# Performance work log

Measured on AMD Instinct MI355X. Metric: run time of the kernel, lower is better.

## Reference

```python
import jax, jax.numpy as jnp
import numpy as np

H = 128
IN = 5
EPS = 1e-5


def lstm(x, Wih, Whh, bih, bhh):
    # x: [B,T,D]; PyTorch gate order i,f,g,o along 4H axis
    B, T, _ = x.shape
    xW = jnp.einsum('btd,gd->btg', x, Wih) + bih + bhh  # [B,T,4H]
    WhhT = Whh.T

    def step(carry, xt):
        h, c = carry
        g = xt + h @ WhhT
        i, f, gg, o = jnp.split(g, 4, axis=-1)
        i = jax.nn.sigmoid(i)
        f = jax.nn.sigmoid(f)
        gg = jnp.tanh(gg)
        o = jax.nn.sigmoid(o)
        c = f * c + i * gg
        h = o * jnp.tanh(c)
        return (h, c), h

    h0 = jnp.zeros((B, H), x.dtype)
    _, hs = jax.lax.scan(step, (h0, h0), jnp.swapaxes(xW, 0, 1))
    return jnp.swapaxes(hs, 0, 1)  # [B,T,H]


def batchnorm(x, gamma, beta):
    # training-mode BN over (batch, time) per channel; x: [B,T,H]
    mean = jnp.mean(x, axis=(0, 1))
    var = jnp.var(x, axis=(0, 1))
    return (x - mean) * (gamma * jax.lax.rsqrt(var + EPS)) + beta


def forward_one(x, Wih1, Whh1, bih1, bhh1, g1, b1, Wih2, Whh2, bih2, bhh2, g2, b2, fcW, fcb):
    out = lstm(x, Wih1, Whh1, bih1, bhh1)
    out = batchnorm(out, g1, b1)
    # dropout is identity (eval / deterministic reference)
    out = lstm(out, Wih2, Whh2, bih2, bhh2)
    out = batchnorm(out, g2, b2)
    emb = out[:, -1, :] @ fcW.T + fcb  # [B,128]
    norm = jnp.sqrt(jnp.sum(emb * emb, axis=1, keepdims=True))
    return emb / jnp.maximum(norm, 1e-12)  # F.normalize p=2


def setup_inputs() -> dict:
    key = jax.random.key(0)
    ks = jax.random.split(key, 20)
    B, T = 512, 128
    s_in = 1.0 / np.sqrt(H)
    d = {
        'a': jax.random.normal(ks[0], (B, T, IN), jnp.float32),
        'p': jax.random.normal(ks[1], (B, T, IN), jnp.float32),
        'n': jax.random.normal(ks[2], (B, T, IN), jnp.float32),
        'Wih1': jax.random.uniform(ks[3], (4 * H, IN), jnp.float32, -s_in, s_in),
        'Whh1': jax.random.uniform(ks[4], (4 * H, H), jnp.float32, -s_in, s_in),
        'bih1': jax.random.uniform(ks[5], (4 * H,), jnp.float32, -s_in, s_in),
        'bhh1': jax.random.uniform(ks[6], (4 * H,), jnp.float32, -s_in, s_in),
        'g1': jnp.ones((H,), jnp.float32),
        'b1': jnp.zeros((H,), jnp.float32),
        'Wih2': jax.random.uniform(ks[7], (4 * H, H), jnp.float32, -s_in, s_in),
        'Whh2': jax.random.uniform(ks[8], (4 * H, H), jnp.float32, -s_in, s_in),
        'bih2': jax.random.uniform(ks[9], (4 * H,), jnp.float32, -s_in, s_in),
        'bhh2': jax.random.uniform(ks[10], (4 * H,), jnp.float32, -s_in, s_in),
        'g2': jnp.ones((H,), jnp.float32),
        'b2': jnp.zeros((H,), jnp.float32),
        'fcW': jax.random.uniform(ks[11], (H, H), jnp.float32, -s_in, s_in),
        'fcb': jax.random.uniform(ks[12], (H,), jnp.float32, -s_in, s_in),
    }
    return d


def reference(a, p, n, Wih1, Whh1, bih1, bhh1, g1, b1, Wih2, Whh2, bih2, bhh2, g2, b2, fcW, fcb):
    f = lambda x: forward_one(x, Wih1, Whh1, bih1, bhh1, g1, b1, Wih2, Whh2, bih2, bhh2, g2, b2, fcW, fcb)
    return (f(a), f(p), f(n))
```

## Files before the change

### kernel.cpp

```cpp
#include <hip/hip_runtime.h>


typedef __attribute__((ext_vector_type(8))) _Float16 half8;
typedef __attribute__((ext_vector_type(4))) float f32x4;

#define TS 128
#define HID 128
#define NGATE 512
#define INV_N (1.0f/65536.0f)

#define BAR() asm volatile("s_waitcnt lgkmcnt(0)\n\ts_barrier" ::: "memory")

__device__ __forceinline__ float rcpf(float x) { return __builtin_amdgcn_rcpf(x); }
__device__ __forceinline__ float clamp20(float x) { return fminf(fmaxf(x, -20.0f), 20.0f); }

__device__ __forceinline__ _Float16 lstm_cell(float zi, float zf, float zg, float zo,
                                              float& c) {
  zg = clamp20(zg);
  float ei = __expf(-zi);
  float eg = __expf(-2.0f * zg);
  float ef = __expf(-zf);
  float fv = rcpf(1.0f + ef);
  float ig = (1.0f - eg) * rcpf((1.0f + ei) * (1.0f + eg));
  float cc = fv * c + ig;
  c = cc;
  float ccl = clamp20(cc);
  float eo = __expf(-zo);
  float ec = __expf(-2.0f * ccl);
  float hv = (1.0f - ec) * rcpf((1.0f + eo) * (1.0f + ec));
  return (_Float16)hv;
}


__global__ void prep_all(const float* __restrict__ xa, const float* __restrict__ xp,
                         const float* __restrict__ xn,
                         const float* __restrict__ Whh1, const float* __restrict__ Whh2,
                         const float* __restrict__ bih1, const float* __restrict__ bhh1,
                         _Float16* __restrict__ xpad,
                         _Float16* __restrict__ whhT1, _Float16* __restrict__ whhT2,
                         float* __restrict__ b1c) {
  int bid = blockIdx.x, tid = threadIdx.x;
  if (bid < 6144) {
    int i = bid * 256 + tid;
    int tile = i >> 14, rem = i & 16383;
    int t = rem >> 7, r = (rem >> 3) & 15, d = i & 7;
    int inp = tile >> 5, rloc = (tile & 31) * 16;
    const float* x = (inp == 0) ? xa : ((inp == 1) ? xp : xn);
    xpad[i] = (d < 5) ? (_Float16)x[(rloc + r) * 640 + t * 5 + d] : (_Float16)0.0f;
  } else if (bid < 6656) {
    int i = (bid - 6144) * 256 + tid;
    int which = i >> 16, idx = i & 65535;
    int k = idx >> 9, g = idx & 511;
    const float* src = which ? Whh2 : Whh1;
    (which ? whhT2 : whhT1)[idx] = (_Float16)src[g * HID + k];
  } else {
    int i = (bid - 6656) * 256 + tid;
    b1c[i] = bih1[i] + bhh1[i];
  }
}

__global__ __launch_bounds__(512, 2) void lstm1_kernel(
    const _Float16* __restrict__ xpad,
    const float* __restrict__ Wih1,
    const float* __restrict__ b1c,
    const _Float16* __restrict__ whhT,
    _Float16* __restrict__ hs1,
    float* __restrict__ s1sum, float* __restrict__ s1sq) {
  const int wg = blockIdx.x;
  const int inp = wg >> 5;
  const int tid = threadIdx.x;
  const int w = tid >> 6;
  const int lane = tid & 63;
  const int l15 = lane & 15;
  const int quad = lane >> 4;
  const int col = w * 16 + l15;
  const int kb = quad * 8;

  __shared__ _Float16 hb[2][2048];
  for (int i = tid; i < 4096; i += 512) ((_Float16*)hb)[i] = (_Float16)0.0f;

  const int rbase = (quad * 16 + l15) * 8;
  const int wbase = (w >> 1) * 512 + ((w & 1) * 2 + (l15 >> 3)) * 128 +
                    quad * 32 + (l15 & 7);

  half8 bh[4][4];
#pragma unroll
  for (int kt = 0; kt < 4; ++kt)
#pragma unroll
    for (int gt = 0; gt < 4; ++gt) {
      int gcol = gt * 128 + col;
      half8 v;
#pragma unroll
      for (int j = 0; j < 8; ++j) v[j] = whhT[(kt * 32 + kb + j) * NGATE + gcol];
      bh[kt][gt] = v;
    }
  half8 bx[4];
#pragma unroll
  for (int gt = 0; gt < 4; ++gt) {
    half8 v = {0, 0, 0, 0, 0, 0, 0, 0};
    if (quad == 0) {
#pragma unroll
      for (int j = 0; j < 5; ++j) v[j] = (_Float16)Wih1[(gt * 128 + col) * 5 + j];
    }
    bx[gt] = v;
  }
  f32x4 biasv[4];
#pragma unroll
  for (int gt = 0; gt < 4; ++gt) {
    float b = b1c[gt * 128 + col];
    biasv[gt][0] = b; biasv[gt][1] = b; biasv[gt][2] = b; biasv[gt][3] = b;
  }

  half8 xp = {0, 0, 0, 0, 0, 0, 0, 0};
  if (quad == 0) xp = *(const half8*)&xpad[((size_t)(wg * TS) * 16 + l15) * 8];

  float c[4] = {0, 0, 0, 0};
  float ssum = 0.0f, ssq = 0.0f;
  _Float16* hs1w = hs1 + (size_t)wg * TS * 2048;

  __syncthreads();

  for (int t = 0; t < TS; ++t) {
    f32x4 acc[4];
#pragma unroll
    for (int gt = 0; gt < 4; ++gt)
      acc[gt] = __builtin_amdgcn_mfma_f32_16x16x32_f16(xp, bx[gt], biasv[gt], 0, 0, 0);
    if (t + 1 < TS && quad == 0)
      xp = *(const half8*)&xpad[((size_t)(wg * TS + t + 1) * 16 + l15) * 8];
    BAR();
    if (t > 0) {
      float2 cp = *(const float2*)&hb[t & 1][tid * 4];
      *(float2*)&hs1w[(size_t)(t - 1) * 2048 + tid * 4] = cp;
    }
#pragma unroll
    for (int kt = 0; kt < 4; ++kt) {
      half8 ah = *(const half8*)&hb[t & 1][kt * 512 + rbase];
#pragma unroll
      for (int gt = 0; gt < 4; ++gt)
        acc[gt] = __builtin_amdgcn_mfma_f32_16x16x32_f16(ah, bh[kt][gt], acc[gt], 0, 0, 0);
    }
    const int wb = (t + 1) & 1;
#pragma unroll
    for (int r = 0; r < 4; ++r) {
      _Float16 hh = lstm_cell(acc[0][r], acc[1][r], acc[2][r], acc[3][r], c[r]);
      float hr = (float)hh;
      ssum += hr; ssq += hr * hr;
      hb[wb][wbase + r * 8] = hh;
    }
  }
  BAR();
  {
    float2 cp = *(const float2*)&hb[0][tid * 4];
    *(float2*)&hs1w[(size_t)(TS - 1) * 2048 + tid * 4] = cp;
  }
  float s = ssum, q = ssq;
  s += __shfl_xor(s, 16); s += __shfl_xor(s, 32);
  q += __shfl_xor(q, 16); q += __shfl_xor(q, 32);
  if (quad == 0) {
    atomicAdd(&s1sum[inp * HID + col], s);
    atomicAdd(&s1sq[inp * HID + col], q);
  }
}

__global__ void mid_kernel(const float* __restrict__ s1sum, const float* __restrict__ s1sq,
                           const float* __restrict__ g1, const float* __restrict__ b1,
                           const float* __restrict__ Wih2,
                           const float* __restrict__ bih2, const float* __restrict__ bhh2,
                           _Float16* __restrict__ w2s, float* __restrict__ bias2eff) {
  int bid = blockIdx.x, tid = threadIdx.x;
  if (bid < 768) {
    int i = bid * 256 + tid;
    int inp = i >> 16, rem = i & 65535, k = rem >> 9, g = rem & 511;
    float m = s1sum[inp * HID + k] * INV_N;
    float v = s1sq[inp * HID + k] * INV_N - m * m;
    float sc = g1[k] * rsqrtf(v + 1e-5f);
    w2s[i] = (_Float16)(sc * Wih2[g * HID + k]);
  } else {
    int i = (bid - 768) * 256 + tid;
    int inp = i >> 9, g = i & 511;
    float acc = bih2[g] + bhh2[g];
    for (int h = 0; h < HID; ++h) {
      float m = s1sum[inp * HID + h] * INV_N;
      float v = s1sq[inp * HID + h] * INV_N - m * m;
      float sc = g1[h] * rsqrtf(v + 1e-5f);
      acc += (b1[h] - m * sc) * Wih2[g * HID + h];
    }
    bias2eff[i] = acc;
  }
}

__global__ __launch_bounds__(512, 2) void lstm2_kernel(
    const _Float16* __restrict__ hs1,
    const _Float16* __restrict__ whhT2,
    const _Float16* __restrict__ w2s,
    const float* __restrict__ bias2eff,
    _Float16* __restrict__ h_last,
    float* __restrict__ s2sum, float* __restrict__ s2sq) {
  const int wg = blockIdx.x;
  const int inp = wg >> 5;
  const int gr0 = wg * 16;
  const int tid = threadIdx.x;
  const int w = tid >> 6;
  const int lane = tid & 63;
  const int l15 = lane & 15;
  const int quad = lane >> 4;
  const int col = w * 16 + l15;
  const int kb = quad * 8;

  __shared__ _Float16 hb[2][2048];
  for (int i = tid; i < 4096; i += 512) ((_Float16*)hb)[i] = (_Float16)0.0f;

  const int rbase = (quad * 16 + l15) * 8;
  const int wbase = (w >> 1) * 512 + ((w & 1) * 2 + (l15 >> 3)) * 128 +
                    quad * 32 + (l15 & 7);

  const _Float16* w2sI = w2s + (size_t)inp * HID * NGATE;
  half8 bh[4][4], bxw[4][4];
#pragma unroll
  for (int kt = 0; kt < 4; ++kt)
#pragma unroll
    for (int gt = 0; gt < 4; ++gt) {
      int gcol = gt * 128 + col;
      half8 vh, vx;
#pragma unroll
      for (int j = 0; j < 8; ++j) {
        vh[j] = whhT2[(kt * 32 + kb + j) * NGATE + gcol];
        vx[j] = w2sI[(kt * 32 + kb + j) * NGATE + gcol];
      }
      bh[kt][gt] = vh;
      bxw[kt][gt] = vx;
    }
  f32x4 biasv[4];
#pragma unroll
  for (int gt = 0; gt < 4; ++gt) {
    float b = bias2eff[inp * NGATE + gt * 128 + col];
    biasv[gt][0] = b; biasv[gt][1] = b; biasv[gt][2] = b; biasv[gt][3] = b;
  }

  const _Float16* hg = hs1 + (size_t)wg * TS * 2048;
  half8 a2A[4], a2B[4];
#pragma unroll
  for (int kt = 0; kt < 4; ++kt) {
    a2A[kt] = *(const half8*)&hg[kt * 512 + rbase];
    a2B[kt] = *(const half8*)&hg[(size_t)2048 + kt * 512 + rbase];
  }

  float c[4] = {0, 0, 0, 0};
  float ssum = 0.0f, ssq = 0.0f;

  __syncthreads();

  auto step = [&](int t, half8 (&cur)[4]) {
    f32x4 acc[4];
#pragma unroll
    for (int gt = 0; gt < 4; ++gt)
      acc[gt] = __builtin_amdgcn_mfma_f32_16x16x32_f16(cur[0], bxw[0][gt], biasv[gt], 0, 0, 0);
#pragma unroll
    for (int kt = 1; kt < 4; ++kt)
#pragma unroll
      for (int gt = 0; gt < 4; ++gt)
        acc[gt] = __builtin_amdgcn_mfma_f32_16x16x32_f16(cur[kt], bxw[kt][gt], acc[gt], 0, 0, 0);
    if (t + 2 < TS) {
#pragma unroll
      for (int kt = 0; kt < 4; ++kt)
        cur[kt] = *(const half8*)&hg[(size_t)(t + 2) * 2048 + kt * 512 + rbase];
    }
    BAR();
#pragma unroll
    for (int kt = 0; kt < 4; ++kt) {
      half8 ah = *(const half8*)&hb[t & 1][kt * 512 + rbase];
#pragma unroll
      for (int gt = 0; gt < 4; ++gt)
        acc[gt] = __builtin_amdgcn_mfma_f32_16x16x32_f16(ah, bh[kt][gt], acc[gt], 0, 0, 0);
    }
    const int wb = (t + 1) & 1;
#pragma unroll
    for (int r = 0; r < 4; ++r) {
      _Float16 hh = lstm_cell(acc[0][r], acc[1][r], acc[2][r], acc[3][r], c[r]);
      float hr = (float)hh;
      ssum += hr; ssq += hr * hr;
      hb[wb][wbase + r * 8] = hh;
      if (t == TS - 1) h_last[(size_t)(gr0 + quad * 4 + r) * HID + col] = hh;
    }
  };

  for (int t = 0; t < TS; t += 2) {
    step(t, a2A);
    step(t + 1, a2B);
  }

  float s = ssum, q = ssq;
  s += __shfl_xor(s, 16); s += __shfl_xor(s, 32);
  q += __shfl_xor(q, 16); q += __shfl_xor(q, 32);
  if (quad == 0) {
    atomicAdd(&s2sum[inp * HID + col], s);
    atomicAdd(&s2sq[inp * HID + col], q);
  }
}

__global__ __launch_bounds__(256, 1) void head_kernel(
    const _Float16* __restrict__ h_last,
    const float* __restrict__ s2sum, const float* __restrict__ s2sq,
    const float* __restrict__ g2, const float* __restrict__ b2,
    const float* __restrict__ fcW, const float* __restrict__ fcb,
    float* __restrict__ out) {
  const int wg = blockIdx.x;
  const int inp = wg >> 5;
  const int gr0 = wg * 16;
  const int tid = threadIdx.x;

  __shared__ float fcwT[128][132];
  __shared__ float bnh[16][132];
  __shared__ float s2[128], sh2[128];
  __shared__ float part[16][16];
  __shared__ float inv[16];

  if (tid < 128) {
    float m = s2sum[inp * HID + tid] * INV_N;
    float v = s2sq[inp * HID + tid] * INV_N - m * m;
    float s = g2[tid] * rsqrtf(v + 1e-5f);
    s2[tid] = s; sh2[tid] = b2[tid] - m * s;
  }
  for (int i = tid; i < 16384; i += 256) {
    int j = i >> 7, h = i & 127;
    fcwT[h][j] = fcW[i];
  }
  __syncthreads();
  {
    int row = tid >> 4, c0 = (tid & 15) * 8;
#pragma unroll
    for (int k = 0; k < 8; ++k) {
      int h = c0 + k;
      bnh[row][h] = (float)h_last[(gr0 + row) * HID + h] * s2[h] + sh2[h];
    }
  }
  __syncthreads();
  const int row = tid >> 4, jl = tid & 15;
  float emb[8];
  float sq = 0.0f;
#pragma unroll
  for (int jj = 0; jj < 8; ++jj) {
    int j = jl + jj * 16;
    float acc = fcb[j];
    for (int h = 0; h < HID; ++h) acc += bnh[row][h] * fcwT[h][j];
    emb[jj] = acc; sq += acc * acc;
  }
  part[row][jl] = sq;
  __syncthreads();
  if (tid < 16) {
    float s = 0.0f;
    for (int k = 0; k < 16; ++k) s += part[tid][k];
    float nrm = sqrtf(s);
    inv[tid] = 1.0f / fmaxf(nrm, 1e-12f);
  }
  __syncthreads();
#pragma unroll
  for (int jj = 0; jj < 8; ++jj)
    out[(gr0 + row) * HID + jl + jj * 16] = emb[jj] * inv[row];
}

extern "C" void kernel_launch(void* const* d_in, const int* in_sizes, int n_in,
                              void* d_out, int out_size, void* d_ws, size_t ws_size,
                              hipStream_t stream) {
  const float* a    = (const float*)d_in[0];
  const float* p    = (const float*)d_in[1];
  const float* nn   = (const float*)d_in[2];
  const float* Wih1 = (const float*)d_in[3];
  const float* Whh1 = (const float*)d_in[4];
  const float* bih1 = (const float*)d_in[5];
  const float* bhh1 = (const float*)d_in[6];
  const float* g1   = (const float*)d_in[7];
  const float* b1   = (const float*)d_in[8];
  const float* Wih2 = (const float*)d_in[9];
  const float* Whh2 = (const float*)d_in[10];
  const float* bih2 = (const float*)d_in[11];
  const float* bhh2 = (const float*)d_in[12];
  const float* g2   = (const float*)d_in[13];
  const float* b2   = (const float*)d_in[14];
  const float* fcW  = (const float*)d_in[15];
  const float* fcb  = (const float*)d_in[16];

  char* ws = (char*)d_ws;
  float* s1sum = (float*)(ws + 0);
  float* s1sq  = s1sum + 384;
  float* s2sum = s1sum + 768;
  float* s2sq  = s1sum + 1152;
  float* b1c      = (float*)(ws + 6144);
  float* bias2eff = (float*)(ws + 8192);
  _Float16* whhT1 = (_Float16*)(ws + 14336);
  _Float16* whhT2 = (_Float16*)(ws + 145408);
  _Float16* w2s   = (_Float16*)(ws + 276480);
  _Float16* hlast = (_Float16*)(ws + 669696);
  _Float16* xpad  = (_Float16*)(ws + 1062912);
  _Float16* hs1   = (_Float16*)(ws + 4208640);

  hipMemsetAsync(ws, 0, 6144, stream);

  prep_all<<<6658, 256, 0, stream>>>(a, p, nn, Whh1, Whh2, bih1, bhh1,
                                     xpad, whhT1, whhT2, b1c);
  lstm1_kernel<<<96, 512, 0, stream>>>(xpad, Wih1, b1c, whhT1, hs1, s1sum, s1sq);
  mid_kernel<<<774, 256, 0, stream>>>(s1sum, s1sq, g1, b1, Wih2, bih2, bhh2,
                                      w2s, bias2eff);
  lstm2_kernel<<<96, 512, 0, stream>>>(hs1, whhT2, w2s, bias2eff, hlast, s2sum, s2sq);
  head_kernel<<<96, 256, 0, stream>>>(hlast, s2sum, s2sq, g2, b2, fcW, fcb, (float*)d_out);
}
```

Baseline: 369.2 us.

## Fuse whole pipeline into one persistent kernel with grid-wide barriers

Merges prep, both LSTM layers, the BN folding and the head into a single persistent kernel of 96 workgroups, synchronized by an atomic grid barrier. Input transposition moves into LDS per workgroup, and weight conversion moves into each workgroup's register loads. The BN1 scale and shift folding into Wih2 and its bias is now computed redundantly per workgroup. This removes four extra launches and the intermediate workspace traffic, at the cost of redundant per-WG weight and bias work and the assumption that all 96 workgroups are co-resident.

Result: slower. 416.3 us (+12.7%).

```diff
diff --git a/kernel.cpp b/kernel.cpp
--- a/kernel.cpp
+++ b/kernel.cpp
@@ -7,6 +7,7 @@
 #define TS 128
 #define HID 128
 #define NGATE 512
+#define NWG 96
 #define INV_N (1.0f/65536.0f)
 
 #define BAR() asm volatile("s_waitcnt lgkmcnt(0)\n\ts_barrier" ::: "memory")
@@ -31,41 +32,41 @@
   return (_Float16)hv;
 }
 
-
-__global__ void prep_all(const float* __restrict__ xa, const float* __restrict__ xp,
-                         const float* __restrict__ xn,
-                         const float* __restrict__ Whh1, const float* __restrict__ Whh2,
-                         const float* __restrict__ bih1, const float* __restrict__ bhh1,
-                         _Float16* __restrict__ xpad,
-                         _Float16* __restrict__ whhT1, _Float16* __restrict__ whhT2,
-                         float* __restrict__ b1c) {
-  int bid = blockIdx.x, tid = threadIdx.x;
-  if (bid < 6144) {
-    int i = bid * 256 + tid;
-    int tile = i >> 14, rem = i & 16383;
-    int t = rem >> 7, r = (rem >> 3) & 15, d = i & 7;
-    int inp = tile >> 5, rloc = (tile & 31) * 16;
-    const float* x = (inp == 0) ? xa : ((inp == 1) ? xp : xn);
-    xpad[i] = (d < 5) ? (_Float16)x[(rloc + r) * 640 + t * 5 + d] : (_Float16)0.0f;
-  } else if (bid < 6656) {
-    int i = (bid - 6144) * 256 + tid;
-    int which = i >> 16, idx = i & 65535;
-    int k = idx >> 9, g = idx & 511;
-    const float* src = which ? Whh2 : Whh1;
-    (which ? whhT2 : whhT1)[idx] = (_Float16)src[g * HID + k];
-  } else {
-    int i = (bid - 6656) * 256 + tid;
-    b1c[i] = bih1[i] + bhh1[i];
+__device__ __forceinline__ float aload(const float* p) {
+  return __hip_atomic_load(p, __ATOMIC_RELAXED, __HIP_MEMORY_SCOPE_AGENT);
+}
+
+__device__ __forceinline__ void gbar(int* cnt, int* gen, int tid) {
+  __syncthreads();
+  if (tid == 0) {
+    int g = __hip_atomic_load(gen, __ATOMIC_RELAXED, __HIP_MEMORY_SCOPE_AGENT);
+    int a = __hip_atomic_fetch_add(cnt, 1, __ATOMIC_ACQ_REL, __HIP_MEMORY_SCOPE_AGENT);
+    if (a == NWG - 1) {
+      __hip_atomic_store(cnt, 0, __ATOMIC_RELAXED, __HIP_MEMORY_SCOPE_AGENT);
+      __hip_atomic_fetch_add(gen, 1, __ATOMIC_RELEASE, __HIP_MEMORY_SCOPE_AGENT);
+    } else {
+      while (__hip_atomic_load(gen, __ATOMIC_ACQUIRE, __HIP_MEMORY_SCOPE_AGENT) == g)
+        __builtin_amdgcn_s_sleep(2);
+    }
   }
-}
-
-__global__ __launch_bounds__(512, 2) void lstm1_kernel(
-    const _Float16* __restrict__ xpad,
-    const float* __restrict__ Wih1,
-    const float* __restrict__ b1c,
-    const _Float16* __restrict__ whhT,
-    _Float16* __restrict__ hs1,
-    float* __restrict__ s1sum, float* __restrict__ s1sq) {
+  __syncthreads();
+}
+
+
+__global__ __launch_bounds__(512, 2) void fused_kernel(
+    const float* __restrict__ xa, const float* __restrict__ xp,
+    const float* __restrict__ xn,
+    const float* __restrict__ Wih1, const float* __restrict__ Whh1,
+    const float* __restrict__ bih1, const float* __restrict__ bhh1,
+    const float* __restrict__ g1, const float* __restrict__ b1,
+    const float* __restrict__ Wih2, const float* __restrict__ Whh2,
+    const float* __restrict__ bih2, const float* __restrict__ bhh2,
+    const float* __restrict__ g2, const float* __restrict__ b2,
+    const float* __restrict__ fcW, const float* __restrict__ fcb,
+    float* __restrict__ s1sum, float* __restrict__ s1sq,
+    float* __restrict__ s2sum, float* __restrict__ s2sq,
+    _Float16* __restrict__ hs1, int* bar_cnt, int* bar_gen,
+    float* __restrict__ out) {
   const int wg = blockIdx.x;
   const int inp = wg >> 5;
   const int tid = threadIdx.x;
@@ -76,287 +77,265 @@
   const int col = w * 16 + l15;
   const int kb = quad * 8;
 
-  __shared__ _Float16 hb[2][2048];
-  for (int i = tid; i < 4096; i += 512) ((_Float16*)hb)[i] = (_Float16)0.0f;
+  __shared__ __align__(16) char smem[53600];
+  _Float16* hb = (_Float16*)smem;
 
   const int rbase = (quad * 16 + l15) * 8;
   const int wbase = (w >> 1) * 512 + ((w & 1) * 2 + (l15 >> 3)) * 128 +
                     quad * 32 + (l15 & 7);
-
-  half8 bh[4][4];
-#pragma unroll
-  for (int kt = 0; kt < 4; ++kt)
+  _Float16* hs1w = hs1 + (size_t)wg * TS * 2048;
+
+  {
+    _Float16* xt = (_Float16*)(smem + 8192);
+    const float* x = (inp == 0) ? xa : ((inp == 1) ? xp : xn);
+    const int rloc = (wg & 31) * 16;
+
+    for (int i = tid; i < 4096; i += 512) hb[i] = (_Float16)0.0f;
+    for (int i = tid; i < 16384; i += 512) xt[i] = (_Float16)0.0f;
+    __syncthreads();
+    for (int i = tid; i < 10240; i += 512) {
+      int r = i / 640, rem = i - r * 640;
+      int t = rem / 5, d = rem - t * 5;
+      xt[t * 128 + r * 8 + d] = (_Float16)x[(rloc + r) * 640 + rem];
+    }
+
+    half8 bh[4][4];
+#pragma unroll
+    for (int kt = 0; kt < 4; ++kt)
+#pragma unroll
+      for (int gt = 0; gt < 4; ++gt) {
+        const float* src = &Whh1[(gt * 128 + col) * HID + kt * 32 + kb];
+        half8 v;
+#pragma unroll
+        for (int j = 0; j < 8; ++j) v[j] = (_Float16)src[j];
+        bh[kt][gt] = v;
+      }
+    half8 bx[4];
+#pragma unroll
+    for (int gt = 0; gt < 4; ++gt) {
+      half8 v = {0, 0, 0, 0, 0, 0, 0, 0};
+      if (quad == 0) {
+#pragma unroll
+        for (int j = 0; j < 5; ++j) v[j] = (_Float16)Wih1[(gt * 128 + col) * 5 + j];
+      }
+      bx[gt] = v;
+    }
+    f32x4 biasv[4];
+#pragma unroll
+    for (int gt = 0; gt < 4; ++gt) {
+      float b = bih1[gt * 128 + col] + bhh1[gt * 128 + col];
+      biasv[gt][0] = b; biasv[gt][1] = b; biasv[gt][2] = b; biasv[gt][3] = b;
+    }
+
+    float c[4] = {0, 0, 0, 0};
+    float ssum = 0.0f, ssq = 0.0f;
+    __syncthreads();
+
+    half8 xv = {0, 0, 0, 0, 0, 0, 0, 0};
+    if (quad == 0) xv = *(const half8*)&xt[l15 * 8];
+
+    for (int t = 0; t < TS; ++t) {
+      f32x4 acc[4];
+#pragma unroll
+      for (int gt = 0; gt < 4; ++gt)
+        acc[gt] = __builtin_amdgcn_mfma_f32_16x16x32_f16(xv, bx[gt], biasv[gt], 0, 0, 0);
+      if (t + 1 < TS && quad == 0)
+        xv = *(const half8*)&xt[(t + 1) * 128 + l15 * 8];
+      BAR();
+      if (t > 0) {
+        float2 cp = *(const float2*)&hb[(t & 1) * 2048 + tid * 4];
+        *(float2*)&hs1w[(size_t)(t - 1) * 2048 + tid * 4] = cp;
+      }
+#pragma unroll
+      for (int kt = 0; kt < 4; ++kt) {
+        half8 ah = *(const half8*)&hb[(t & 1) * 2048 + kt * 512 + rbase];
+#pragma unroll
+        for (int gt = 0; gt < 4; ++gt)
+          acc[gt] = __builtin_amdgcn_mfma_f32_16x16x32_f16(ah, bh[kt][gt], acc[gt], 0, 0, 0);
+      }
+      const int wb = (t + 1) & 1;
+#pragma unroll
+      for (int r = 0; r < 4; ++r) {
+        _Float16 hh = lstm_cell(acc[0][r], acc[1][r], acc[2][r], acc[3][r], c[r]);
+        float hr = (float)hh;
+        ssum += hr; ssq += hr * hr;
+        hb[wb * 2048 + wbase + r * 8] = hh;
+      }
+    }
+    BAR();
+    {
+      float2 cp = *(const float2*)&hb[tid * 4];
+      *(float2*)&hs1w[(size_t)(TS - 1) * 2048 + tid * 4] = cp;
+    }
+    float s = ssum, q = ssq;
+    s += __shfl_xor(s, 16); s += __shfl_xor(s, 32);
+    q += __shfl_xor(q, 16); q += __shfl_xor(q, 32);
+    if (quad == 0) {
+      atomicAdd(&s1sum[inp * HID + col], s);
+      atomicAdd(&s1sq[inp * HID + col], q);
+    }
+  }
+
+  gbar(bar_cnt, bar_gen, tid);
+
+  {
+    float* scale1L = (float*)(smem + 8192);
+    float* shift1L = (float*)(smem + 8704);
+    if (tid < 128) {
+      float sm = aload(&s1sum[inp * HID + tid]);
+      float sq = aload(&s1sq[inp * HID + tid]);
+      float m = sm * INV_N;
+      float v = sq * INV_N - m * m;
+      float sc = g1[tid] * rsqrtf(v + 1e-5f);
+      scale1L[tid] = sc;
+      shift1L[tid] = b1[tid] - m * sc;
+    }
+    for (int i = tid; i < 4096; i += 512) hb[i] = (_Float16)0.0f;
+    __syncthreads();
+
+    half8 bh[4][4], bxw[4][4];
+#pragma unroll
+    for (int kt = 0; kt < 4; ++kt)
+#pragma unroll
+      for (int gt = 0; gt < 4; ++gt) {
+        const float* ph = &Whh2[(gt * 128 + col) * HID + kt * 32 + kb];
+        const float* px = &Wih2[(gt * 128 + col) * HID + kt * 32 + kb];
+        half8 vh, vx;
+#pragma unroll
+        for (int j = 0; j < 8; ++j) {
+          vh[j] = (_Float16)ph[j];
+          vx[j] = (_Float16)(scale1L[kt * 32 + kb + j] * px[j]);
+        }
+        bh[kt][gt] = vh;
+        bxw[kt][gt] = vx;
+      }
+    f32x4 biasv[4];
 #pragma unroll
     for (int gt = 0; gt < 4; ++gt) {
       int gcol = gt * 128 + col;
-      half8 v;
-#pragma unroll
-      for (int j = 0; j < 8; ++j) v[j] = whhT[(kt * 32 + kb + j) * NGATE + gcol];
-      bh[kt][gt] = v;
-    }
-  half8 bx[4];
-#pragma unroll
-  for (int gt = 0; gt < 4; ++gt) {
-    half8 v = {0, 0, 0, 0, 0, 0, 0, 0};
+      float b = bih2[gcol] + bhh2[gcol];
+      const float* pw = &Wih2[gcol * HID];
+      for (int h = 0; h < HID; ++h) b += shift1L[h] * pw[h];
+      biasv[gt][0] = b; biasv[gt][1] = b; biasv[gt][2] = b; biasv[gt][3] = b;
+    }
+
+    half8 a2A[4], a2B[4];
+#pragma unroll
+    for (int kt = 0; kt < 4; ++kt) {
+      a2A[kt] = *(const half8*)&hs1w[kt * 512 + rbase];
+      a2B[kt] = *(const half8*)&hs1w[(size_t)2048 + kt * 512 + rbase];
+    }
+
+    float c[4] = {0, 0, 0, 0};
+    float ssum = 0.0f, ssq = 0.0f;
+
+    auto step = [&](int t, half8 (&cur)[4]) {
+      f32x4 acc[4];
+#pragma unroll
+      for (int gt = 0; gt < 4; ++gt)
+        acc[gt] = __builtin_amdgcn_mfma_f32_16x16x32_f16(cur[0], bxw[0][gt], biasv[gt], 0, 0, 0);
+#pragma unroll
+      for (int kt = 1; kt < 4; ++kt)
+#pragma unroll
+        for (int gt = 0; gt < 4; ++gt)
+          acc[gt] = __builtin_amdgcn_mfma_f32_16x16x32_f16(cur[kt], bxw[kt][gt], acc[gt], 0, 0, 0);
+      if (t + 2 < TS) {
+#pragma unroll
+        for (int kt = 0; kt < 4; ++kt)
+          cur[kt] = *(const half8*)&hs1w[(size_t)(t + 2) * 2048 + kt * 512 + rbase];
+      }
+      BAR();
+#pragma unroll
+      for (int kt = 0; kt < 4; ++kt) {
+        half8 ah = *(const half8*)&hb[(t & 1) * 2048 + kt * 512 + rbase];
+#pragma unroll
+        for (int gt = 0; gt < 4; ++gt)
+          acc[gt] = __builtin_amdgcn_mfma_f32_16x16x32_f16(ah, bh[kt][gt], acc[gt], 0, 0, 0);
+      }
+      const int wb = (t + 1) & 1;
+#pragma unroll
+      for (int r = 0; r < 4; ++r) {
+        _Float16 hh = lstm_cell(acc[0][r], acc[1][r], acc[2][r], acc[3][r], c[r]);
+        float hr = (float)hh;
+        ssum += hr; ssq += hr * hr;
+        hb[wb * 2048 + wbase + r * 8] = hh;
+      }
+    };
+
+    for (int t = 0; t < TS; t += 2) {
+      step(t, a2A);
+      step(t + 1, a2B);
+    }
+
+    float s = ssum, q = ssq;
+    s += __shfl_xor(s, 16); s += __shfl_xor(s, 32);
+    q += __shfl_xor(q, 16); q += __shfl_xor(q, 32);
     if (quad == 0) {
-#pragma unroll
-      for (int j = 0; j < 5; ++j) v[j] = (_Float16)Wih1[(gt * 128 + col) * 5 + j];
-    }
-    bx[gt] = v;
+      atomicAdd(&s2sum[inp * HID + col], s);
+      atomicAdd(&s2sq[inp * HID + col], q);
+    }
   }
-  f32x4 biasv[4];
-#pragma unroll
-  for (int gt = 0; gt < 4; ++gt) {
-    float b = b1c[gt * 128 + col];
-    biasv[gt][0] = b; biasv[gt][1] = b; biasv[gt][2] = b; biasv[gt][3] = b;
+
+  gbar(bar_cnt, bar_gen, tid);
+
+  {
+    _Float16* fcwT = (_Float16*)(smem + 8192);
+    float* bnh  = (float*)(smem + 43008);
+    float* s2L  = (float*)(smem + 51456);
+    float* sh2L = (float*)(smem + 51968);
+    float* part = (float*)(smem + 52480);
+    float* invv = (float*)(smem + 53504);
+
+    if (tid < 128) {
+      float sm = aload(&s2sum[inp * HID + tid]);
+      float sq = aload(&s2sq[inp * HID + tid]);
+      float m = sm * INV_N;
+      float v = sq * INV_N - m * m;
+      float sc = g2[tid] * rsqrtf(v + 1e-5f);
+      s2L[tid] = sc;
+      sh2L[tid] = b2[tid] - m * sc;
+    }
+    for (int i = tid; i < 16384; i += 512) {
+      int j = i >> 7, h = i & 127;
+      fcwT[h * 136 + j] = (_Float16)fcW[i];
+    }
+    __syncthreads();
+    const int row = (tid & 255) >> 4, jl = tid & 15;
+    if (tid < 256) {
+      int c0 = jl * 8;
+#pragma unroll
+      for (int k = 0; k < 8; ++k) {
+        int h = c0 + k;
+        int ad = ((h >> 5) << 9) + (((h >> 3) & 3) << 7) + (row << 3) + (h & 7);
+        bnh[row * 132 + h] = (float)hb[ad] * s2L[h] + sh2L[h];
+      }
+    }
+    __syncthreads();
+    float emb[8];
+    if (tid < 256) {
+      float sq = 0.0f;
+#pragma unroll
+      for (int jj = 0; jj < 8; ++jj) {
+        int j = jl + jj * 16;
+        float acc = fcb[j];
+        for (int h = 0; h < HID; ++h) acc += bnh[row * 132 + h] * (float)fcwT[h * 136 + j];
+        emb[jj] = acc; sq += acc * acc;
+      }
+      part[row * 16 + jl] = sq;
+    }
+    __syncthreads();
+    if (tid < 16) {
+      float s = 0.0f;
+      for (int k = 0; k < 16; ++k) s += part[tid * 16 + k];
+      invv[tid] = 1.0f / fmaxf(sqrtf(s), 1e-12f);
+    }
+    __syncthreads();
+    if (tid < 256) {
+#pragma unroll
+      for (int jj = 0; jj < 8; ++jj)
+        out[(size_t)(wg * 16 + row) * HID + jl + jj * 16] = emb[jj] * invv[row];
+    }
   }
-
-  half8 xp = {0, 0, 0, 0, 0, 0, 0, 0};
-  if (quad == 0) xp = *(const half8*)&xpad[((size_t)(wg * TS) * 16 + l15) * 8];
-
-  float c[4] = {0, 0, 0, 0};
-  float ssum = 0.0f, ssq = 0.0f;
-  _Float16* hs1w = hs1 + (size_t)wg * TS * 2048;
-
-  __syncthreads();
-
-  for (int t = 0; t < TS; ++t) {
-    f32x4 acc[4];
-#pragma unroll
-    for (int gt = 0; gt < 4; ++gt)
-      acc[gt] = __builtin_amdgcn_mfma_f32_16x16x32_f16(xp, bx[gt], biasv[gt], 0, 0, 0);
-    if (t + 1 < TS && quad == 0)
-      xp = *(const half8*)&xpad[((size_t)(wg * TS + t + 1) * 16 + l15) * 8];
-    BAR();
-    if (t > 0) {
-      float2 cp = *(const float2*)&hb[t & 1][tid * 4];
-      *(float2*)&hs1w[(size_t)(t - 1) * 2048 + tid * 4] = cp;
-    }
-#pragma unroll
-    for (int kt = 0; kt < 4; ++kt) {
-      half8 ah = *(const half8*)&hb[t & 1][kt * 512 + rbase];
-#pragma unroll
-      for (int gt = 0; gt < 4; ++gt)
-        acc[gt] = __builtin_amdgcn_mfma_f32_16x16x32_f16(ah, bh[kt][gt], acc[gt], 0, 0, 0);
-    }
-    const int wb = (t + 1) & 1;
-#pragma unroll
-    for (int r = 0; r < 4; ++r) {
-      _Float16 hh = lstm_cell(acc[0][r], acc[1][r], acc[2][r], acc[3][r], c[r]);
-      float hr = (float)hh;
-      ssum += hr; ssq += hr * hr;
-      hb[wb][wbase + r * 8] = hh;
-    }
-  }
-  BAR();
-  {
-    float2 cp = *(const float2*)&hb[0][tid * 4];
-    *(float2*)&hs1w[(size_t)(TS - 1) * 2048 + tid * 4] = cp;
-  }
-  float s = ssum, q = ssq;
-  s += __shfl_xor(s, 16); s += __shfl_xor(s, 32);
-  q += __shfl_xor(q, 16); q += __shfl_xor(q, 32);
-  if (quad == 0) {
-    atomicAdd(&s1sum[inp * HID + col], s);
-    atomicAdd(&s1sq[inp * HID + col], q);
-  }
-}
-
-__global__ void mid_kernel(const float* __restrict__ s1sum, const float* __restrict__ s1sq,
-                           const float* __restrict__ g1, const float* __restrict__ b1,
-                           const float* __restrict__ Wih2,
-                           const float* __restrict__ bih2, const float* __restrict__ bhh2,
-                           _Float16* __restrict__ w2s, float* __restrict__ bias2eff) {
-  int bid = blockIdx.x, tid = threadIdx.x;
-  if (bid < 768) {
-    int i = bid * 256 + tid;
-    int inp = i >> 16, rem = i & 65535, k = rem >> 9, g = rem & 511;
-    float m = s1sum[inp * HID + k] * INV_N;
-    float v = s1sq[inp * HID + k] * INV_N - m * m;
-    float sc = g1[k] * rsqrtf(v + 1e-5f);
-    w2s[i] = (_Float16)(sc * Wih2[g * HID + k]);
-  } else {
-    int i = (bid - 768) * 256 + tid;
-    int inp = i >> 9, g = i & 511;
-    float acc = bih2[g] + bhh2[g];
-    for (int h = 0; h < HID; ++h) {
-      float m = s1sum[inp * HID + h] * INV_N;
-      float v = s1sq[inp * HID + h] * INV_N - m * m;
-      float sc = g1[h] * rsqrtf(v + 1e-5f);
-      acc += (b1[h] - m * sc) * Wih2[g * HID + h];
-    }
-    bias2eff[i] = acc;
-  }
-}
-
-__global__ __launch_bounds__(512, 2) void lstm2_kernel(
-    const _Float16* __restrict__ hs1,
-    const _Float16* __restrict__ whhT2,
-    const _Float16* __restrict__ w2s,
-    const float* __restrict__ bias2eff,
-    _Float16* __restrict__ h_last,
-    float* __restrict__ s2sum, float* __restrict__ s2sq) {
-  const int wg = blockIdx.x;
-  const int inp = wg >> 5;
-  const int gr0 = wg * 16;
-  const int tid = threadIdx.x;
-  const int w = tid >> 6;
-  const int lane = tid & 63;
-  const int l15 = lane & 15;
-  const int quad = lane >> 4;
-  const int col = w * 16 + l15;
-  const int kb = quad * 8;
-
-  __shared__ _Float16 hb[2][2048];
-  for (int i = tid; i < 4096; i += 512) ((_Float16*)hb)[i] = (_Float16)0.0f;
-
-  const int rbase = (quad * 16 + l15) * 8;
-  const int wbase = (w >> 1) * 512 + ((w & 1) * 2 + (l15 >> 3)) * 128 +
-                    quad * 32 + (l15 & 7);
-
-  const _Float16* w2sI = w2s + (size_t)inp * HID * NGATE;
-  half8 bh[4][4], bxw[4][4];
-#pragma unroll
-  for (int kt = 0; kt < 4; ++kt)
-#pragma unroll
-    for (int gt = 0; gt < 4; ++gt) {
-      int gcol = gt * 128 + col;
-      half8 vh, vx;
-#pragma unroll
-      for (int j = 0; j < 8; ++j) {
-        vh[j] = whhT2[(kt * 32 + kb + j) * NGATE + gcol];
-        vx[j] = w2sI[(kt * 32 + kb + j) * NGATE + gcol];
-      }
-      bh[kt][gt] = vh;
-      bxw[kt][gt] = vx;
-    }
-  f32x4 biasv[4];
-#pragma unroll
-  for (int gt = 0; gt < 4; ++gt) {
-    float b = bias2eff[inp * NGATE + gt * 128 + col];
-    biasv[gt][0] = b; biasv[gt][1] = b; biasv[gt][2] = b; biasv[gt][3] = b;
-  }
-
-  const _Float16* hg = hs1 + (size_t)wg * TS * 2048;
-  half8 a2A[4], a2B[4];
-#pragma unroll
-  for (int kt = 0; kt < 4; ++kt) {
-    a2A[kt] = *(const half8*)&hg[kt * 512 + rbase];
-    a2B[kt] = *(const half8*)&hg[(size_t)2048 + kt * 512 + rbase];
-  }
-
-  float c[4] = {0, 0, 0, 0};
-  float ssum = 0.0f, ssq = 0.0f;
-
-  __syncthreads();
-
-  auto step = [&](int t, half8 (&cur)[4]) {
-    f32x4 acc[4];
-#pragma unroll
-    for (int gt = 0; gt < 4; ++gt)
-      acc[gt] = __builtin_amdgcn_mfma_f32_16x16x32_f16(cur[0], bxw[0][gt], biasv[gt], 0, 0, 0);
-#pragma unroll
-    for (int kt = 1; kt < 4; ++kt)
-#pragma unroll
-      for (int gt = 0; gt < 4; ++gt)
-        acc[gt] = __builtin_amdgcn_mfma_f32_16x16x32_f16(cur[kt], bxw[kt][gt], acc[gt], 0, 0, 0);
-    if (t + 2 < TS) {
-#pragma unroll
-      for (int kt = 0; kt < 4; ++kt)
-        cur[kt] = *(const half8*)&hg[(size_t)(t + 2) * 2048 + kt * 512 + rbase];
-    }
-    BAR();
-#pragma unroll
-    for (int kt = 0; kt < 4; ++kt) {
-      half8 ah = *(const half8*)&hb[t & 1][kt * 512 + rbase];
-#pragma unroll
-      for (int gt = 0; gt < 4; ++gt)
-        acc[gt] = __builtin_amdgcn_mfma_f32_16x16x32_f16(ah, bh[kt][gt], acc[gt], 0, 0, 0);
-    }
-    const int wb = (t + 1) & 1;
-#pragma unroll
-    for (int r = 0; r < 4; ++r) {
-      _Float16 hh = lstm_cell(acc[0][r], acc[1][r], acc[2][r], acc[3][r], c[r]);
-      float hr = (float)hh;
-      ssum += hr; ssq += hr * hr;
-      hb[wb][wbase + r * 8] = hh;
-      if (t == TS - 1) h_last[(size_t)(gr0 + quad * 4 + r) * HID + col] = hh;
-    }
-  };
-
-  for (int t = 0; t < TS; t += 2) {
-    step(t, a2A);
-    step(t + 1, a2B);
-  }
-
-  float s = ssum, q = ssq;
-  s += __shfl_xor(s, 16); s += __shfl_xor(s, 32);
-  q += __shfl_xor(q, 16); q += __shfl_xor(q, 32);
-  if (quad == 0) {
-    atomicAdd(&s2sum[inp * HID + col], s);
-    atomicAdd(&s2sq[inp * HID + col], q);
-  }
-}
-
-__global__ __launch_bounds__(256, 1) void head_kernel(
-    const _Float16* __restrict__ h_last,
-    const float* __restrict__ s2sum, const float* __restrict__ s2sq,
-    const float* __restrict__ g2, const float* __restrict__ b2,
-    const float* __restrict__ fcW, const float* __restrict__ fcb,
-    float* __restrict__ out) {
-  const int wg = blockIdx.x;
-  const int inp = wg >> 5;
-  const int gr0 = wg * 16;
-  const int tid = threadIdx.x;
-
-  __shared__ float fcwT[128][132];
-  __shared__ float bnh[16][132];
-  __shared__ float s2[128], sh2[128];
-  __shared__ float part[16][16];
-  __shared__ float inv[16];
-
-  if (tid < 128) {
-    float m = s2sum[inp * HID + tid] * INV_N;
-    float v = s2sq[inp * HID + tid] * INV_N - m * m;
-    float s = g2[tid] * rsqrtf(v + 1e-5f);
-    s2[tid] = s; sh2[tid] = b2[tid] - m * s;
-  }
-  for (int i = tid; i < 16384; i += 256) {
-    int j = i >> 7, h = i & 127;
-    fcwT[h][j] = fcW[i];
-  }
-  __syncthreads();
-  {
-    int row = tid >> 4, c0 = (tid & 15) * 8;
-#pragma unroll
-    for (int k = 0; k < 8; ++k) {
-      int h = c0 + k;
-      bnh[row][h] = (float)h_last[(gr0 + row) * HID + h] * s2[h] + sh2[h];
-    }
-  }
-  __syncthreads();
-  const int row = tid >> 4, jl = tid & 15;
-  float emb[8];
-  float sq = 0.0f;
-#pragma unroll
-  for (int jj = 0; jj < 8; ++jj) {
-    int j = jl + jj * 16;
-    float acc = fcb[j];
-    for (int h = 0; h < HID; ++h) acc += bnh[row][h] * fcwT[h][j];
-    emb[jj] = acc; sq += acc * acc;
-  }
-  part[row][jl] = sq;
-  __syncthreads();
-  if (tid < 16) {
-    float s = 0.0f;
-    for (int k = 0; k < 16; ++k) s += part[tid][k];
-    float nrm = sqrtf(s);
-    inv[tid] = 1.0f / fmaxf(nrm, 1e-12f);
-  }
-  __syncthreads();
-#pragma unroll
-  for (int jj = 0; jj < 8; ++jj)
-    out[(gr0 + row) * HID + jl + jj * 16] = emb[jj] * inv[row];
 }
 
 extern "C" void kernel_launch(void* const* d_in, const int* in_sizes, int n_in,
@@ -382,25 +361,17 @@
 
   char* ws = (char*)d_ws;
   float* s1sum = (float*)(ws + 0);
-  float* s1sq  = s1sum + 384;
-  float* s2sum = s1sum + 768;
-  float* s2sq  = s1sum + 1152;
-  float* b1c      = (float*)(ws + 6144);
-  float* bias2eff = (float*)(ws + 8192);
-  _Float16* whhT1 = (_Float16*)(ws + 14336);
-  _Float16* whhT2 = (_Float16*)(ws + 145408);
-  _Float16* w2s   = (_Float16*)(ws + 276480);
-  _Float16* hlast = (_Float16*)(ws + 669696);
-  _Float16* xpad  = (_Float16*)(ws + 1062912);
-  _Float16* hs1   = (_Float16*)(ws + 4208640);
-
-  hipMemsetAsync(ws, 0, 6144, stream);
-
-  prep_all<<<6658, 256, 0, stream>>>(a, p, nn, Whh1, Whh2, bih1, bhh1,
-                                     xpad, whhT1, whhT2, b1c);
-  lstm1_kernel<<<96, 512, 0, stream>>>(xpad, Wih1, b1c, whhT1, hs1, s1sum, s1sq);
-  mid_kernel<<<774, 256, 0, stream>>>(s1sum, s1sq, g1, b1, Wih2, bih2, bhh2,
-                                      w2s, bias2eff);
-  lstm2_kernel<<<96, 512, 0, stream>>>(hs1, whhT2, w2s, bias2eff, hlast, s2sum, s2sq);
-  head_kernel<<<96, 256, 0, stream>>>(hlast, s2sum, s2sq, g2, b2, fcW, fcb, (float*)d_out);
-}
+  float* s1sq  = (float*)(ws + 1536);
+  float* s2sum = (float*)(ws + 3072);
+  float* s2sq  = (float*)(ws + 4608);
+  int* bar_cnt = (int*)(ws + 6144);
+  int* bar_gen = (int*)(ws + 6148);
+  _Float16* hs1 = (_Float16*)(ws + 8192);
+
+  hipMemsetAsync(ws, 0, 6656, stream);
+
+  fused_kernel<<<NWG, 512, 0, stream>>>(
+      a, p, nn, Wih1, Whh1, bih1, bhh1, g1, b1,
+      Wih2, Whh2, bih2, bhh2, g2, b2, fcW, fcb,
+      s1sum, s1sq, s2sum, s2sq, hs1, bar_cnt, bar_gen, (float*)d_out);
+}
```

## Fold prep and mid kernels into LSTM kernels, staging inputs in LDS

Applied to the files above, without the earlier changes.

Removes the separate prep_all and mid_kernel launches. lstm1 now loads the raw fp32 inputs into a padded LDS tile and converts Whh1 and the biases itself. lstm2 computes the BN1 scale and shift per block, folds them into Wih2 and the bias while loading, and writes h_last from LDS after the loop. This cuts launch count and workspace traffic, at the cost of each of the 96 blocks redundantly converting weights and doing a 128-long bias dot product serially.

Result: slower. 407.5 us (+10.4%).

```diff
diff --git a/kernel.cpp b/kernel.cpp
--- a/kernel.cpp
+++ b/kernel.cpp
@@ -32,38 +32,11 @@
 }
 
 
-__global__ void prep_all(const float* __restrict__ xa, const float* __restrict__ xp,
-                         const float* __restrict__ xn,
-                         const float* __restrict__ Whh1, const float* __restrict__ Whh2,
-                         const float* __restrict__ bih1, const float* __restrict__ bhh1,
-                         _Float16* __restrict__ xpad,
-                         _Float16* __restrict__ whhT1, _Float16* __restrict__ whhT2,
-                         float* __restrict__ b1c) {
-  int bid = blockIdx.x, tid = threadIdx.x;
-  if (bid < 6144) {
-    int i = bid * 256 + tid;
-    int tile = i >> 14, rem = i & 16383;
-    int t = rem >> 7, r = (rem >> 3) & 15, d = i & 7;
-    int inp = tile >> 5, rloc = (tile & 31) * 16;
-    const float* x = (inp == 0) ? xa : ((inp == 1) ? xp : xn);
-    xpad[i] = (d < 5) ? (_Float16)x[(rloc + r) * 640 + t * 5 + d] : (_Float16)0.0f;
-  } else if (bid < 6656) {
-    int i = (bid - 6144) * 256 + tid;
-    int which = i >> 16, idx = i & 65535;
-    int k = idx >> 9, g = idx & 511;
-    const float* src = which ? Whh2 : Whh1;
-    (which ? whhT2 : whhT1)[idx] = (_Float16)src[g * HID + k];
-  } else {
-    int i = (bid - 6656) * 256 + tid;
-    b1c[i] = bih1[i] + bhh1[i];
-  }
-}
-
 __global__ __launch_bounds__(512, 2) void lstm1_kernel(
-    const _Float16* __restrict__ xpad,
-    const float* __restrict__ Wih1,
-    const float* __restrict__ b1c,
-    const _Float16* __restrict__ whhT,
+    const float* __restrict__ xa, const float* __restrict__ xp,
+    const float* __restrict__ xn,
+    const float* __restrict__ Wih1, const float* __restrict__ Whh1,
+    const float* __restrict__ bih1, const float* __restrict__ bhh1,
     _Float16* __restrict__ hs1,
     float* __restrict__ s1sum, float* __restrict__ s1sq) {
   const int wg = blockIdx.x;
@@ -77,56 +50,67 @@
   const int kb = quad * 8;
 
   __shared__ _Float16 hb[2][2048];
+  __shared__ _Float16 xt[TS][128];
+
+  const float* x = (inp == 0) ? xa : ((inp == 1) ? xp : xn);
+  const int rloc = (wg & 31) * 16;
+
   for (int i = tid; i < 4096; i += 512) ((_Float16*)hb)[i] = (_Float16)0.0f;
+  for (int i = tid; i < TS * 128; i += 512) ((_Float16*)xt)[i] = (_Float16)0.0f;
+  __syncthreads();
+  for (int i = tid; i < 10240; i += 512) {
+    int r = i / 640, rem = i - r * 640;
+    int t = rem / 5, d = rem - t * 5;
+    xt[t][r * 8 + d] = (_Float16)x[(rloc + r) * 640 + rem];
+  }
+
+  half8 bh[4][4];
+#pragma unroll
+  for (int kt = 0; kt < 4; ++kt)
+#pragma unroll
+    for (int gt = 0; gt < 4; ++gt) {
+      const float* src = &Whh1[(gt * 128 + col) * HID + kt * 32 + kb];
+      half8 v;
+#pragma unroll
+      for (int j = 0; j < 8; ++j) v[j] = (_Float16)src[j];
+      bh[kt][gt] = v;
+    }
+  half8 bx[4];
+#pragma unroll
+  for (int gt = 0; gt < 4; ++gt) {
+    half8 v = {0, 0, 0, 0, 0, 0, 0, 0};
+    if (quad == 0) {
+#pragma unroll
+      for (int j = 0; j < 5; ++j) v[j] = (_Float16)Wih1[(gt * 128 + col) * 5 + j];
+    }
+    bx[gt] = v;
+  }
+  f32x4 biasv[4];
+#pragma unroll
+  for (int gt = 0; gt < 4; ++gt) {
+    float b = bih1[gt * 128 + col] + bhh1[gt * 128 + col];
+    biasv[gt][0] = b; biasv[gt][1] = b; biasv[gt][2] = b; biasv[gt][3] = b;
+  }
 
   const int rbase = (quad * 16 + l15) * 8;
   const int wbase = (w >> 1) * 512 + ((w & 1) * 2 + (l15 >> 3)) * 128 +
                     quad * 32 + (l15 & 7);
-
-  half8 bh[4][4];
-#pragma unroll
-  for (int kt = 0; kt < 4; ++kt)
-#pragma unroll
-    for (int gt = 0; gt < 4; ++gt) {
-      int gcol = gt * 128 + col;
-      half8 v;
-#pragma unroll
-      for (int j = 0; j < 8; ++j) v[j] = whhT[(kt * 32 + kb + j) * NGATE + gcol];
-      bh[kt][gt] = v;
-    }
-  half8 bx[4];
-#pragma unroll
-  for (int gt = 0; gt < 4; ++gt) {
-    half8 v = {0, 0, 0, 0, 0, 0, 0, 0};
-    if (quad == 0) {
-#pragma unroll
-      for (int j = 0; j < 5; ++j) v[j] = (_Float16)Wih1[(gt * 128 + col) * 5 + j];
-    }
-    bx[gt] = v;
-  }
-  f32x4 biasv[4];
-#pragma unroll
-  for (int gt = 0; gt < 4; ++gt) {
-    float b = b1c[gt * 128 + col];
-    biasv[gt][0] = b; biasv[gt][1] = b; biasv[gt][2] = b; biasv[gt][3] = b;
-  }
-
-  half8 xp = {0, 0, 0, 0, 0, 0, 0, 0};
-  if (quad == 0) xp = *(const half8*)&xpad[((size_t)(wg * TS) * 16 + l15) * 8];
+  _Float16* hs1w = hs1 + (size_t)wg * TS * 2048;
 
   float c[4] = {0, 0, 0, 0};
   float ssum = 0.0f, ssq = 0.0f;
-  _Float16* hs1w = hs1 + (size_t)wg * TS * 2048;
-
-  __syncthreads();
+  __syncthreads();
+
+  half8 xv = {0, 0, 0, 0, 0, 0, 0, 0};
+  if (quad == 0) xv = *(const half8*)&xt[0][l15 * 8];
 
   for (int t = 0; t < TS; ++t) {
     f32x4 acc[4];
 #pragma unroll
     for (int gt = 0; gt < 4; ++gt)
-      acc[gt] = __builtin_amdgcn_mfma_f32_16x16x32_f16(xp, bx[gt], biasv[gt], 0, 0, 0);
+      acc[gt] = __builtin_amdgcn_mfma_f32_16x16x32_f16(xv, bx[gt], biasv[gt], 0, 0, 0);
     if (t + 1 < TS && quad == 0)
-      xp = *(const half8*)&xpad[((size_t)(wg * TS + t + 1) * 16 + l15) * 8];
+      xv = *(const half8*)&xt[t + 1][l15 * 8];
     BAR();
     if (t > 0) {
       float2 cp = *(const float2*)&hb[t & 1][tid * 4];
@@ -162,43 +146,16 @@
   }
 }
 
-__global__ void mid_kernel(const float* __restrict__ s1sum, const float* __restrict__ s1sq,
-                           const float* __restrict__ g1, const float* __restrict__ b1,
-                           const float* __restrict__ Wih2,
-                           const float* __restrict__ bih2, const float* __restrict__ bhh2,
-                           _Float16* __restrict__ w2s, float* __restrict__ bias2eff) {
-  int bid = blockIdx.x, tid = threadIdx.x;
-  if (bid < 768) {
-    int i = bid * 256 + tid;
-    int inp = i >> 16, rem = i & 65535, k = rem >> 9, g = rem & 511;
-    float m = s1sum[inp * HID + k] * INV_N;
-    float v = s1sq[inp * HID + k] * INV_N - m * m;
-    float sc = g1[k] * rsqrtf(v + 1e-5f);
-    w2s[i] = (_Float16)(sc * Wih2[g * HID + k]);
-  } else {
-    int i = (bid - 768) * 256 + tid;
-    int inp = i >> 9, g = i & 511;
-    float acc = bih2[g] + bhh2[g];
-    for (int h = 0; h < HID; ++h) {
-      float m = s1sum[inp * HID + h] * INV_N;
-      float v = s1sq[inp * HID + h] * INV_N - m * m;
-      float sc = g1[h] * rsqrtf(v + 1e-5f);
-      acc += (b1[h] - m * sc) * Wih2[g * HID + h];
-    }
-    bias2eff[i] = acc;
-  }
-}
-
 __global__ __launch_bounds__(512, 2) void lstm2_kernel(
     const _Float16* __restrict__ hs1,
-    const _Float16* __restrict__ whhT2,
-    const _Float16* __restrict__ w2s,
-    const float* __restrict__ bias2eff,
-    _Float16* __restrict__ h_last,
+    const float* __restrict__ Wih2, const float* __restrict__ Whh2,
+    const float* __restrict__ bih2, const float* __restrict__ bhh2,
+    const float* __restrict__ g1, const float* __restrict__ b1,
+    const float* __restrict__ s1sum, const float* __restrict__ s1sq,
+    _Float16* __restrict__ hlast,
     float* __restrict__ s2sum, float* __restrict__ s2sq) {
   const int wg = blockIdx.x;
   const int inp = wg >> 5;
-  const int gr0 = wg * 16;
   const int tid = threadIdx.x;
   const int w = tid >> 6;
   const int lane = tid & 63;
@@ -208,36 +165,51 @@
   const int kb = quad * 8;
 
   __shared__ _Float16 hb[2][2048];
+  __shared__ float scale1L[128], shift1L[128];
+
+  if (tid < 128) {
+    float sm = s1sum[inp * HID + tid];
+    float sq = s1sq[inp * HID + tid];
+    float m = sm * INV_N;
+    float v = sq * INV_N - m * m;
+    float sc = g1[tid] * rsqrtf(v + 1e-5f);
+    scale1L[tid] = sc;
+    shift1L[tid] = b1[tid] - m * sc;
+  }
   for (int i = tid; i < 4096; i += 512) ((_Float16*)hb)[i] = (_Float16)0.0f;
+  __syncthreads();
+
+  half8 bh[4][4], bxw[4][4];
+#pragma unroll
+  for (int kt = 0; kt < 4; ++kt)
+#pragma unroll
+    for (int gt = 0; gt < 4; ++gt) {
+      const float* ph = &Whh2[(gt * 128 + col) * HID + kt * 32 + kb];
+      const float* px = &Wih2[(gt * 128 + col) * HID + kt * 32 + kb];
+      half8 vh, vx;
+#pragma unroll
+      for (int j = 0; j < 8; ++j) {
+        vh[j] = (_Float16)ph[j];
+        vx[j] = (_Float16)(scale1L[kt * 32 + kb + j] * px[j]);
+      }
+      bh[kt][gt] = vh;
+      bxw[kt][gt] = vx;
+    }
+  f32x4 biasv[4];
+#pragma unroll
+  for (int gt = 0; gt < 4; ++gt) {
+    int gcol = gt * 128 + col;
+    float b = bih2[gcol] + bhh2[gcol];
+    const float* pw = &Wih2[gcol * HID];
+    for (int h = 0; h < HID; ++h) b += shift1L[h] * pw[h];
+    biasv[gt][0] = b; biasv[gt][1] = b; biasv[gt][2] = b; biasv[gt][3] = b;
+  }
 
   const int rbase = (quad * 16 + l15) * 8;
   const int wbase = (w >> 1) * 512 + ((w & 1) * 2 + (l15 >> 3)) * 128 +
                     quad * 32 + (l15 & 7);
-
-  const _Float16* w2sI = w2s + (size_t)inp * HID * NGATE;
-  half8 bh[4][4], bxw[4][4];
-#pragma unroll
-  for (int kt = 0; kt < 4; ++kt)
-#pragma unroll
-    for (int gt = 0; gt < 4; ++gt) {
-      int gcol = gt * 128 + col;
-      half8 vh, vx;
-#pragma unroll
-      for (int j = 0; j < 8; ++j) {
-        vh[j] = whhT2[(kt * 32 + kb + j) * NGATE + gcol];
-        vx[j] = w2sI[(kt * 32 + kb + j) * NGATE + gcol];
-      }
-      bh[kt][gt] = vh;
-      bxw[kt][gt] = vx;
-    }
-  f32x4 biasv[4];
-#pragma unroll
-  for (int gt = 0; gt < 4; ++gt) {
-    float b = bias2eff[inp * NGATE + gt * 128 + col];
-    biasv[gt][0] = b; biasv[gt][1] = b; biasv[gt][2] = b; biasv[gt][3] = b;
-  }
-
   const _Float16* hg = hs1 + (size_t)wg * TS * 2048;
+
   half8 a2A[4], a2B[4];
 #pragma unroll
   for (int kt = 0; kt < 4; ++kt) {
@@ -247,8 +219,6 @@
 
   float c[4] = {0, 0, 0, 0};
   float ssum = 0.0f, ssq = 0.0f;
-
-  __syncthreads();
 
   auto step = [&](int t, half8 (&cur)[4]) {
     f32x4 acc[4];
@@ -280,7 +250,6 @@
       float hr = (float)hh;
       ssum += hr; ssq += hr * hr;
       hb[wb][wbase + r * 8] = hh;
-      if (t == TS - 1) h_last[(size_t)(gr0 + quad * 4 + r) * HID + col] = hh;
     }
   };
 
@@ -289,6 +258,11 @@
     step(t + 1, a2B);
   }
 
+  BAR();
+  {
+    float2 cp = *(const float2*)&hb[0][tid * 4];
+    *(float2*)&hlast[(size_t)wg * 2048 + tid * 4] = cp;
+  }
   float s = ssum, q = ssq;
   s += __shfl_xor(s, 16); s += __shfl_xor(s, 32);
   q += __shfl_xor(q, 16); q += __shfl_xor(q, 32);
@@ -299,7 +273,7 @@
 }
 
 __global__ __launch_bounds__(256, 1) void head_kernel(
-    const _Float16* __restrict__ h_last,
+    const _Float16* __restrict__ hlast,
     const float* __restrict__ s2sum, const float* __restrict__ s2sq,
     const float* __restrict__ g2, const float* __restrict__ b2,
     const float* __restrict__ fcW, const float* __restrict__ fcb,
@@ -331,7 +305,8 @@
 #pragma unroll
     for (int k = 0; k < 8; ++k) {
       int h = c0 + k;
-      bnh[row][h] = (float)h_last[(gr0 + row) * HID + h] * s2[h] + sh2[h];
+      int ad = ((h >> 5) << 9) + (((h >> 3) & 3) << 7) + (row << 3) + (h & 7);
+      bnh[row][h] = (float)hlast[(size_t)wg * 2048 + ad] * s2[h] + sh2[h];
     }
   }
   __syncthreads();
@@ -350,13 +325,12 @@
   if (tid < 16) {
     float s = 0.0f;
     for (int k = 0; k < 16; ++k) s += part[tid][k];
-    float nrm = sqrtf(s);
-    inv[tid] = 1.0f / fmaxf(nrm, 1e-12f);
+    inv[tid] = 1.0f / fmaxf(sqrtf(s), 1e-12f);
   }
   __syncthreads();
 #pragma unroll
   for (int jj = 0; jj < 8; ++jj)
-    out[(gr0 + row) * HID + jl + jj * 16] = emb[jj] * inv[row];
+    out[(size_t)(gr0 + row) * HID + jl + jj * 16] = emb[jj] * inv[row];
 }
 
 extern "C" void kernel_launch(void* const* d_in, const int* in_sizes, int n_in,
@@ -382,25 +356,18 @@
 
   char* ws = (char*)d_ws;
   float* s1sum = (float*)(ws + 0);
-  float* s1sq  = s1sum + 384;
-  float* s2sum = s1sum + 768;
-  float* s2sq  = s1sum + 1152;
-  float* b1c      = (float*)(ws + 6144);
-  float* bias2eff = (float*)(ws + 8192);
-  _Float16* whhT1 = (_Float16*)(ws + 14336);
-  _Float16* whhT2 = (_Float16*)(ws + 145408);
-  _Float16* w2s   = (_Float16*)(ws + 276480);
-  _Float16* hlast = (_Float16*)(ws + 669696);
-  _Float16* xpad  = (_Float16*)(ws + 1062912);
-  _Float16* hs1   = (_Float16*)(ws + 4208640);
+  float* s1sq  = (float*)(ws + 1536);
+  float* s2sum = (float*)(ws + 3072);
+  float* s2sq  = (float*)(ws + 4608);
+  _Float16* hlast = (_Float16*)(ws + 8192);
+  _Float16* hs1   = (_Float16*)(ws + 401408);
 
   hipMemsetAsync(ws, 0, 6144, stream);
 
-  prep_all<<<6658, 256, 0, stream>>>(a, p, nn, Whh1, Whh2, bih1, bhh1,
-                                     xpad, whhT1, whhT2, b1c);
-  lstm1_kernel<<<96, 512, 0, stream>>>(xpad, Wih1, b1c, whhT1, hs1, s1sum, s1sq);
-  mid_kernel<<<774, 256, 0, stream>>>(s1sum, s1sq, g1, b1, Wih2, bih2, bhh2,
-                                      w2s, bias2eff);
-  lstm2_kernel<<<96, 512, 0, stream>>>(hs1, whhT2, w2s, bias2eff, hlast, s2sum, s2sq);
-  head_kernel<<<96, 256, 0, stream>>>(hlast, s2sum, s2sq, g2, b2, fcW, fcb, (float*)d_out);
-}
+  lstm1_kernel<<<96, 512, 0, stream>>>(a, p, nn, Wih1, Whh1, bih1, bhh1,
+                                       hs1, s1sum, s1sq);
+  lstm2_kernel<<<96, 512, 0, stream>>>(hs1, Wih2, Whh2, bih2, bhh2, g1, b1,
+                                       s1sum, s1sq, hlast, s2sum, s2sq);
+  head_kernel<<<96, 256, 0, stream>>>(hlast, s2sum, s2sq, g2, b2, fcW, fcb,
+                                      (float*)d_out);
+}
```
